# Kernel tuning notes

Hardware: AMD Instinct MI355X
Metric: run time of the kernel (lower is better)

Reference implementation:

```python
import jax, jax.numpy as jnp
import numpy as np

SLOPE = 25.0  # snntorch surrogate.fast_sigmoid default slope
THR = 1.0
BETA = 0.5
NUM_HEADS = 8

@jax.custom_vjp
def spike(u):
    # forward: heaviside; backward: fast-sigmoid surrogate
    return (u > 0).astype(u.dtype)

def _spike_fwd(u):
    return (u > 0).astype(u.dtype), u

def _spike_bwd(u, g):
    return (g / (SLOPE * jnp.abs(u) + 1.0) ** 2,)

spike.defvjp(_spike_fwd, _spike_bwd)

def lif(inp, mem):
    # snntorch Leaky, reset_mechanism='subtract': reset from previous mem (detached)
    reset = jax.lax.stop_gradient((mem > THR).astype(mem.dtype))
    mem_new = BETA * mem + inp - reset * THR
    spk = spike(mem_new - THR)
    return spk, mem_new

def conv1x1(x, W):
    # nn.Conv2d(C,C,1,bias=False): pure channel matmul
    return jnp.einsum('bihw,oi->bohw', x, W)

def setup_inputs():
    key = jax.random.key(0)
    ks = jax.random.split(key, 5)
    B, C, H, W = 8, 256, 64, 64
    x = jax.random.normal(ks[0], (B, C, H, W), jnp.float32)
    z = jnp.zeros((B, C, H, W), jnp.float32)
    s = 1.0 / np.sqrt(C)
    Wq = jax.random.normal(ks[1], (C, C), jnp.float32) * s
    Wk = jax.random.normal(ks[2], (C, C), jnp.float32) * s
    Wv = jax.random.normal(ks[3], (C, C), jnp.float32) * s
    Wo = jax.random.normal(ks[4], (C, C), jnp.float32) * s
    gamma = jnp.ones((C,), jnp.float32)
    beta_bn = jnp.zeros((C,), jnp.float32)
    return {'x': x, 'q_mem': z, 'k_mem': z, 'v_mem': z,
            'Wq': Wq, 'Wk': Wk, 'Wv': Wv, 'Wo': Wo,
            'gamma': gamma, 'beta_bn': beta_bn}

def reference(x, q_mem, k_mem, v_mem, Wq, Wk, Wv, Wo, gamma, beta_bn):
    B, C, H, W = x.shape
    N = H * W
    hd = C // NUM_HEADS
    scale = hd ** -0.5

    q_spk, q_mem_n = lif(conv1x1(x, Wq), q_mem)
    k_spk, k_mem_n = lif(conv1x1(x, Wk), k_mem)
    v_spk, v_mem_n = lif(conv1x1(x, Wv), v_mem)

    # bipolar spikes in {-1,+1}, reshape to (B, h, N, d)
    def to_heads(s):
        t = (2.0 * s - 1.0).reshape(B, NUM_HEADS, hd, N)
        return jnp.transpose(t, (0, 1, 3, 2))

    q = jax.nn.elu(to_heads(q_spk)) + 1.0
    k = jax.nn.elu(to_heads(k_spk)) + 1.0
    v = to_heads(v_spk)

    kv = jnp.einsum('bhnd,bhne->bhde', k, v)            # (B,h,d,d)
    out = jnp.einsum('bhnd,bhde->bhne', q, kv) * scale  # (B,h,N,d)
    k_sum = jnp.sum(k, axis=2)                          # (B,h,d)
    denom = jnp.einsum('bhnd,bhd->bhn', q, k_sum) + 1e-6
    out = out / denom[..., None]

    out = jnp.transpose(out, (0, 1, 3, 2)).reshape(B, C, H, W)
    out = conv1x1(out, Wo)

    # BatchNorm2d, training mode (biased batch stats), eps=1e-5
    mean = jnp.mean(out, axis=(0, 2, 3), keepdims=True)
    var = jnp.var(out, axis=(0, 2, 3), keepdims=True)
    out = (out - mean) / jnp.sqrt(var + 1e-5)
    out = out * gamma[None, :, None, None] + beta_bn[None, :, None, None]

    return (out, q_mem_n, k_mem_n, v_mem_n)
```

## Files before the change

### kernel.cpp

```cpp
#include <hip/hip_runtime.h>

#define B_ 8
#define C_ 256
#define N_ 4096
#define HD_ 32

#define ALPHA_ 0.36787944117144233f
#define BETAS_ (2.0f - ALPHA_)
#define SCALE_ 0.17677669529663687f

typedef _Float16 f16;
typedef _Float16 f16x8 __attribute__((ext_vector_type(8)));
typedef float f32x4 __attribute__((ext_vector_type(4)));

#define MFMA(a,b,c) __builtin_amdgcn_mfma_f32_16x16x32_f16((a),(b),(c),0,0,0)

#define GLDS(g, l) __builtin_amdgcn_global_load_lds( \
    (const __attribute__((address_space(1))) void*)(g), \
    (__attribute__((address_space(3))) void*)(l), 16, 0, 0)

__global__ __launch_bounds__(256) void transpose_split(
    const float* __restrict__ x, f16* __restrict__ XTh, f16* __restrict__ XTl)
{
    __shared__ float tile[32][257];
    int t = threadIdx.x;
    int b = blockIdx.z, i0 = blockIdx.y * 32, n0 = blockIdx.x * 256;
    const float* src = x + ((size_t)b * C_ + i0) * N_ + n0;
    int r = t >> 3, c0 = (t & 7) * 32;
    #pragma unroll
    for (int q = 0; q < 8; ++q) {
        float4 v = *reinterpret_cast<const float4*>(src + (size_t)r * N_ + c0 + q * 4);
        tile[r][c0 + q*4 + 0] = v.x; tile[r][c0 + q*4 + 1] = v.y;
        tile[r][c0 + q*4 + 2] = v.z; tile[r][c0 + q*4 + 3] = v.w;
    }
    __syncthreads();
    size_t ob = ((size_t)b * N_ + n0 + t) * C_ + i0;
    #pragma unroll
    for (int q = 0; q < 4; ++q) {
        f16x8 hv, lv;
        #pragma unroll
        for (int j = 0; j < 8; ++j) {
            float v = tile[q*8 + j][t];
            f16 h = (f16)v;
            hv[j] = h;
            lv[j] = (f16)(v - (float)h);
        }
        *reinterpret_cast<f16x8*>(XTh + ob + q*8) = hv;
        *reinterpret_cast<f16x8*>(XTl + ob + q*8) = lv;
    }
}

__global__ __launch_bounds__(256) void weight_split(
    const float* __restrict__ Wq, const float* __restrict__ Wk,
    const float* __restrict__ Wv, const float* __restrict__ Wo,
    f16* __restrict__ Wch, f16* __restrict__ Wcl)
{
    int idx4 = (blockIdx.x * 256 + threadIdx.x) * 4;
    int o = idx4 >> 8, i = idx4 & 255;
    const float* src = (o < 256) ? (Wq + (size_t)o * 256)
                     : (o < 512) ? (Wk + (size_t)(o - 256) * 256)
                     : (o < 768) ? (Wv + (size_t)(o - 512) * 256)
                                 : (Wo + (size_t)(o - 768) * 256);
    float4 v = *reinterpret_cast<const float4*>(src + i);
    f16 h0 = (f16)v.x, h1 = (f16)v.y, h2 = (f16)v.z, h3 = (f16)v.w;
    f16 hh[4] = { h0, h1, h2, h3 };
    f16 ll[4] = { (f16)(v.x - (float)h0), (f16)(v.y - (float)h1),
                  (f16)(v.z - (float)h2), (f16)(v.w - (float)h3) };
    *reinterpret_cast<uint2*>(Wch + idx4) = *reinterpret_cast<uint2*>(hh);
    *reinterpret_cast<uint2*>(Wcl + idx4) = *reinterpret_cast<uint2*>(ll);
}

template<int Y, bool LIF>
__global__ __launch_bounds__(256, 2) void mfma_gemm(
    const f16* __restrict__ Wch, const f16* __restrict__ Wcl,
    const f16* __restrict__ Bh,  const f16* __restrict__ Bl,
    const float* __restrict__ mq, const float* __restrict__ mk2,
    const float* __restrict__ mv,
    float* __restrict__ o0, float* __restrict__ o1, float* __restrict__ o2)
{
    int gid = blockIdx.x;
    int xcd = gid & 7, slot = gid >> 3;
    int y = slot % Y, gl = slot / Y;
    int b = xcd, xt = gl;
    int oBase = (LIF ? 0 : 768) + y * 128;
    int nT = xt * 256;

    const float* memP = nullptr; float* outP; int chBase;
    if (LIF) {
        int conv = y >> 1;
        memP = (conv == 0) ? mq : (conv == 1) ? mk2 : mv;
        outP = (conv == 0) ? o0 : (conv == 1) ? o1 : o2;
        chBase = (y & 1) * 128;
    } else { outP = o0; chBase = y * 128; }

    __shared__ f16 sm[3072 * 8];

    int t = threadIdx.x;
    int wid = t >> 6, lane = t & 63;
    int wm = wid >> 1, wn = wid & 1;
    int lr = lane & 15, g = lane >> 4;

    const f16* g0[12];
    #pragma unroll
    for (int i = 0; i < 12; ++i) {
        int s = wid * 768 + i * 64 + lane;
        const f16* gp;
        if (s < 512) {
            int r = s >> 2, c = (s & 3) ^ ((r >> 1) & 3);
            gp = Wch + (size_t)(oBase + r) * 256 + c * 8;
        } else if (s < 1024) {
            int s2 = s - 512; int r = s2 >> 2, c = (s2 & 3) ^ ((r >> 1) & 3);
            gp = Wcl + (size_t)(oBase + r) * 256 + c * 8;
        } else if (s < 2048) {
            int s2 = s - 1024; int r = s2 >> 2, c = (s2 & 3) ^ ((r >> 1) & 3);
            gp = Bh + ((size_t)b * N_ + nT + r) * 256 + c * 8;
        } else {
            int s2 = s - 2048; int r = s2 >> 2, c = (s2 & 3) ^ ((r >> 1) & 3);
            gp = Bl + ((size_t)b * N_ + nT + r) * 256 + c * 8;
        }
        g0[i] = gp;
    }

    f32x4 acc[4][8];
    #pragma unroll
    for (int m = 0; m < 4; ++m)
        #pragma unroll
        for (int n = 0; n < 8; ++n) acc[m][n] = (f32x4){0.f, 0.f, 0.f, 0.f};

    for (int k0 = 0; k0 < 256; k0 += 32) {
        #pragma unroll
        for (int i = 0; i < 12; ++i) {
            int s = wid * 768 + i * 64 + lane;
            GLDS(g0[i] + k0, &sm[s * 8]);
        }
        __syncthreads();

        f16x8 ah[4], al[4];
        #pragma unroll
        for (int m = 0; m < 4; ++m) {
            int r = wm * 64 + m * 16 + lr;
            int sw = g ^ ((r >> 1) & 3);
            ah[m] = *reinterpret_cast<const f16x8*>(&sm[(r * 4 + sw) * 8]);
            al[m] = *reinterpret_cast<const f16x8*>(&sm[(512 + r * 4 + sw) * 8]);
        }
        #pragma unroll
        for (int n = 0; n < 8; ++n) {
            int r = wn * 128 + n * 16 + lr;
            int sw = g ^ ((r >> 1) & 3);
            f16x8 bh8 = *reinterpret_cast<const f16x8*>(&sm[(1024 + r * 4 + sw) * 8]);
            f16x8 bl8 = *reinterpret_cast<const f16x8*>(&sm[(2048 + r * 4 + sw) * 8]);
            #pragma unroll
            for (int m = 0; m < 4; ++m) {
                acc[m][n] = MFMA(ah[m], bh8, acc[m][n]);
                acc[m][n] = MFMA(ah[m], bl8, acc[m][n]);
                acc[m][n] = MFMA(al[m], bh8, acc[m][n]);
            }
        }
        __syncthreads();
    }

    #pragma unroll
    for (int m = 0; m < 4; ++m) {
        int oLoc = chBase + wm * 64 + m * 16 + g * 4;
        #pragma unroll
        for (int n = 0; n < 8; ++n) {
            int nn = nT + wn * 128 + n * 16 + lr;
            #pragma unroll
            for (int r = 0; r < 4; ++r) {
                size_t idx = ((size_t)b * C_ + oLoc + r) * N_ + nn;
                float v = acc[m][n][r];
                if (LIF) {
                    float mm = memP[idx];
                    outP[idx] = 0.5f * mm + v - (mm > 1.0f ? 1.0f : 0.0f);
                } else {
                    outP[idx] = v;
                }
            }
        }
    }
}

__global__ __launch_bounds__(256) void kv_stage1(
    const float* __restrict__ Km, const float* __restrict__ Vm,
    int* __restrict__ pkv, int* __restrict__ pck, int* __restrict__ pcv)
{
    int bh = blockIdx.x, sl = blockIdx.y;
    int b = bh >> 3, h = bh & 7;
    const float* Kp = Km + ((size_t)(b * C_ + h * HD_)) * N_ + sl * 512;
    const float* Vp = Vm + ((size_t)(b * C_ + h * HD_)) * N_ + sl * 512;

    __shared__ unsigned long long mk[32][9], mv[32][9];
    int t = threadIdx.x, wave = t >> 6, lane = t & 63;

    for (int r = wave; r < 32; r += 4) {
        const float* kr = Kp + (size_t)r * N_;
        const float* vr = Vp + (size_t)r * N_;
        #pragma unroll
        for (int seg = 0; seg < 2; ++seg) {
            float4 kf = *reinterpret_cast<const float4*>(kr + seg * 256 + lane * 4);
            float4 vf = *reinterpret_cast<const float4*>(vr + seg * 256 + lane * 4);
            unsigned long long k0 = __ballot(kf.x > 1.0f);
            unsigned long long k1 = __ballot(kf.y > 1.0f);
            unsigned long long k2 = __ballot(kf.z > 1.0f);
            unsigned long long k3 = __ballot(kf.w > 1.0f);
            unsigned long long v0 = __ballot(vf.x > 1.0f);
            unsigned long long v1 = __ballot(vf.y > 1.0f);
            unsigned long long v2 = __ballot(vf.z > 1.0f);
            unsigned long long v3 = __ballot(vf.w > 1.0f);
            if (lane == 0) {
                mk[r][seg*4+0] = k0; mk[r][seg*4+1] = k1;
                mk[r][seg*4+2] = k2; mk[r][seg*4+3] = k3;
                mv[r][seg*4+0] = v0; mv[r][seg*4+1] = v1;
                mv[r][seg*4+2] = v2; mv[r][seg*4+3] = v3;
            }
        }
    }
    __syncthreads();

    int base = (bh * 8 + sl);
    int d = t >> 3, e0 = (t & 7) * 4;
    #pragma unroll
    for (int j = 0; j < 4; ++j) {
        int e = e0 + j, P = 0;
        #pragma unroll
        for (int w = 0; w < 8; ++w) P += __popcll(mk[d][w] & mv[e][w]);
        pkv[(size_t)base * 1024 + d * 32 + e] = P;
    }
    if (t < 32) {
        int c = 0;
        #pragma unroll
        for (int w = 0; w < 8; ++w) c += __popcll(mk[t][w]);
        pck[base * 32 + t] = c;
    } else if (t < 64) {
        int dd = t - 32, c = 0;
        #pragma unroll
        for (int w = 0; w < 8; ++w) c += __popcll(mv[dd][w]);
        pcv[base * 32 + dd] = c;
    }
}

__global__ __launch_bounds__(256) void kv_stage2(
    const int* __restrict__ pkv, const int* __restrict__ pck,
    const int* __restrict__ pcv, float* __restrict__ kvp, float* __restrict__ ksump)
{
    int bh = blockIdx.x, t = threadIdx.x;
    __shared__ float ck[32], cv[32];
    if (t < 32) {
        int s = 0;
        #pragma unroll
        for (int sl = 0; sl < 8; ++sl) s += pck[(bh * 8 + sl) * 32 + t];
        ck[t] = (float)s;
    } else if (t < 64) {
        int dd = t - 32, s = 0;
        #pragma unroll
        for (int sl = 0; sl < 8; ++sl) s += pcv[(bh * 8 + sl) * 32 + dd];
        cv[dd] = (float)s;
    }
    __syncthreads();
    int d = t >> 3, e0 = (t & 7) * 4;
    #pragma unroll
    for (int j = 0; j < 4; ++j) {
        int e = e0 + j, P = 0;
        #pragma unroll
        for (int sl = 0; sl < 8; ++sl) P += pkv[(size_t)(bh * 8 + sl) * 1024 + d * 32 + e];
        float skv = 2.0f * (float)P - ck[d];
        float sv  = 2.0f * cv[e] - 4096.0f;
        kvp[(size_t)bh * 1024 + d * 32 + e] = ALPHA_ * sv + BETAS_ * skv;
    }
    if ((t & 7) == 0)
        ksump[bh * 32 + d] = ALPHA_ * 4096.0f + BETAS_ * ck[d];
}

__global__ __launch_bounds__(256) void att_kernel(
    const float* __restrict__ Qm, const float* __restrict__ kvp,
    const float* __restrict__ ksump, f16* __restrict__ ATh, f16* __restrict__ ATl)
{
    int bh = blockIdx.y; int b = bh >> 3, h = bh & 7;
    int n0 = blockIdx.x * 256;
    const float* Qp = Qm + ((size_t)(b * C_ + h * HD_)) * N_;

    __shared__ float qs[32][260];
    int t = threadIdx.x;
    {
        int r  = t >> 3, c0 = (t & 7) * 32;
        #pragma unroll
        for (int q4 = 0; q4 < 8; ++q4) {
            float4 v = *reinterpret_cast<const float4*>(&Qp[(size_t)r * N_ + n0 + c0 + q4 * 4]);
            qs[r][c0 + q4*4 + 0] = (v.x > 1.0f) ? 2.0f : ALPHA_;
            qs[r][c0 + q4*4 + 1] = (v.y > 1.0f) ? 2.0f : ALPHA_;
            qs[r][c0 + q4*4 + 2] = (v.z > 1.0f) ? 2.0f : ALPHA_;
            qs[r][c0 + q4*4 + 3] = (v.w > 1.0f) ? 2.0f : ALPHA_;
        }
    }
    __syncthreads();

    float q[32];
    #pragma unroll
    for (int d2 = 0; d2 < 32; ++d2) q[d2] = qs[d2][t];

    const float* ksb = ksump + bh * 32;
    float den = 1e-6f;
    #pragma unroll
    for (int d2 = 0; d2 < 32; ++d2) den += q[d2] * ksb[d2];
    float rden = SCALE_ / den;

    const float* kvb = kvp + (size_t)bh * 1024;
    size_t ob = ((size_t)b * N_ + n0 + t) * C_ + h * HD_;
    #pragma unroll
    for (int qq = 0; qq < 4; ++qq) {
        f16x8 hv, lv;
        #pragma unroll
        for (int j = 0; j < 8; ++j) {
            int e = qq * 8 + j;
            float num = 0.0f;
            #pragma unroll
            for (int d2 = 0; d2 < 32; ++d2) num += q[d2] * kvb[d2 * 32 + e];
            float val = num * rden;
            f16 hh = (f16)val;
            hv[j] = hh;
            lv[j] = (f16)(val - (float)hh);
        }
        *reinterpret_cast<f16x8*>(ATh + ob + qq * 8) = hv;
        *reinterpret_cast<f16x8*>(ATl + ob + qq * 8) = lv;
    }
}

__global__ __launch_bounds__(1024) void bn_stats(
    const float* __restrict__ out2, float* __restrict__ stats)
{
    int o = blockIdx.x, t = threadIdx.x;
    double s = 0.0, ss = 0.0;
    for (int b = 0; b < B_; ++b) {
        const float* p = out2 + ((size_t)b * C_ + o) * N_;
        float4 v = *reinterpret_cast<const float4*>(&p[t * 4]);
        s  += (double)v.x + (double)v.y + (double)v.z + (double)v.w;
        ss += (double)v.x * v.x + (double)v.y * v.y + (double)v.z * v.z + (double)v.w * v.w;
    }
    __shared__ double rs[1024], rss[1024];
    rs[t] = s; rss[t] = ss;
    __syncthreads();
    for (int st = 512; st > 0; st >>= 1) {
        if (t < st) { rs[t] += rs[t + st]; rss[t] += rss[t + st]; }
        __syncthreads();
    }
    if (t == 0) {
        double mean = rs[0] / 32768.0;
        double var  = rss[0] / 32768.0 - mean * mean;
        stats[o * 2 + 0] = (float)mean;
        stats[o * 2 + 1] = (float)(1.0 / sqrt(var + 1e-5));
    }
}

__global__ __launch_bounds__(256) void bn_apply(
    float* __restrict__ out, const float* __restrict__ stats,
    const float* __restrict__ gamma, const float* __restrict__ beta)
{
    size_t i = ((size_t)blockIdx.x * 256 + threadIdx.x) * 4;
    int o = (int)((i >> 12) & 255);
    float m = stats[o * 2], r = stats[o * 2 + 1];
    float g = gamma[o] * r;
    float c = beta[o] - m * g;
    float4 v = *reinterpret_cast<float4*>(&out[i]);
    v.x = v.x * g + c; v.y = v.y * g + c;
    v.z = v.z * g + c; v.w = v.w * g + c;
    *reinterpret_cast<float4*>(&out[i]) = v;
}

extern "C" void kernel_launch(void* const* d_in, const int* in_sizes, int n_in,
                              void* d_out, int out_size, void* d_ws, size_t ws_size,
                              hipStream_t stream)
{
    (void)in_sizes; (void)n_in; (void)out_size; (void)ws_size;

    const float* x     = (const float*)d_in[0];
    const float* qmem  = (const float*)d_in[1];
    const float* kmem  = (const float*)d_in[2];
    const float* vmem  = (const float*)d_in[3];
    const float* Wq    = (const float*)d_in[4];
    const float* Wk    = (const float*)d_in[5];
    const float* Wv    = (const float*)d_in[6];
    const float* Wo    = (const float*)d_in[7];
    const float* gamma = (const float*)d_in[8];
    const float* beta  = (const float*)d_in[9];

    const size_t TSZ = (size_t)B_ * C_ * N_;
    float* out0 = (float*)d_out;
    float* outq = out0 + TSZ;
    float* outk = outq + TSZ;
    float* outv = outk + TSZ;

    char* w = (char*)d_ws;
    f16* XTh = (f16*)w;           w += TSZ * 2;
    f16* XTl = (f16*)w;           w += TSZ * 2;
    f16* ATh = (f16*)w;           w += TSZ * 2;
    f16* ATl = (f16*)w;           w += TSZ * 2;
    f16* Wch = (f16*)w;           w += 1024 * 256 * 2;
    f16* Wcl = (f16*)w;           w += 1024 * 256 * 2;
    int* pkv = (int*)w;           w += 64 * 8 * 1024 * 4;
    int* pck = (int*)w;           w += 64 * 8 * 32 * 4;
    int* pcv = (int*)w;           w += 64 * 8 * 32 * 4;
    float* kvp   = (float*)w;     w += 64 * 1024 * 4;
    float* ksump = (float*)w;     w += 64 * 32 * 4;
    float* stats = (float*)w;     w += 256 * 2 * 4;

    dim3 blk(256);

    transpose_split<<<dim3(16, 8, 8), blk, 0, stream>>>(x, XTh, XTl);
    weight_split<<<dim3(256), blk, 0, stream>>>(Wq, Wk, Wv, Wo, Wch, Wcl);

    mfma_gemm<6, true><<<dim3(768), blk, 0, stream>>>(
        Wch, Wcl, XTh, XTl, qmem, kmem, vmem, outq, outk, outv);

    kv_stage1<<<dim3(64, 8), blk, 0, stream>>>(outk, outv, pkv, pck, pcv);
    kv_stage2<<<dim3(64), blk, 0, stream>>>(pkv, pck, pcv, kvp, ksump);

    att_kernel<<<dim3(16, 64), blk, 0, stream>>>(outq, kvp, ksump, ATh, ATl);

    mfma_gemm<2, false><<<dim3(256), blk, 0, stream>>>(
        Wch, Wcl, ATh, ATl, nullptr, nullptr, nullptr, out0, nullptr, nullptr);

    bn_stats<<<dim3(256), dim3(1024), 0, stream>>>(out0, stats);
    bn_apply<<<dim3(8192), blk, 0, stream>>>(out0, stats, gamma, beta);
}
```

Baseline: 184.6 us.

## Double-buffer LDS in split-f16 MFMA GEMM and retile to 256x128 with 512 threads

The GEMM kernel now keeps two LDS buffers and issues global-to-LDS loads for the next K slice while computing on the current one, which removes one barrier per iteration and hides load latency. The tile shape changes from 128 output channels x 256 pixels with 256 threads to 256 channels x 128 pixels with 512 threads (8 waves), halving each wave's accumulator count. The grid mapping changes accordingly (one conv per y). In exchange, LDS use doubles to about 96KB per block, so only one block fits per CU. The loop also still has a trailing barrier, and whether the single barrier is enough to guard the buffer being overwritten depends on how it is placed.

```diff
diff --git a/kernel.cpp b/kernel.cpp
--- a/kernel.cpp
+++ b/kernel.cpp
@@ -71,7 +71,7 @@
 }
 
 template<int Y, bool LIF>
-__global__ __launch_bounds__(256, 2) void mfma_gemm(
+__global__ __launch_bounds__(512, 1) void mfma_gemm(
     const f16* __restrict__ Wch, const f16* __restrict__ Wcl,
     const f16* __restrict__ Bh,  const f16* __restrict__ Bl,
     const float* __restrict__ mq, const float* __restrict__ mk2,
@@ -79,76 +79,83 @@
     float* __restrict__ o0, float* __restrict__ o1, float* __restrict__ o2)
 {
     int gid = blockIdx.x;
-    int xcd = gid & 7, slot = gid >> 3;
-    int y = slot % Y, gl = slot / Y;
-    int b = xcd, xt = gl;
-    int oBase = (LIF ? 0 : 768) + y * 128;
-    int nT = xt * 256;
-
-    const float* memP = nullptr; float* outP; int chBase;
+    int b = gid & 7, slot = gid >> 3;
+    int y = slot % Y, nt = slot / Y;
+    int oBase = LIF ? y * 256 : 768;
+    int nT = nt * 128;
+
+    const float* memP = nullptr; float* outP;
     if (LIF) {
-        int conv = y >> 1;
-        memP = (conv == 0) ? mq : (conv == 1) ? mk2 : mv;
-        outP = (conv == 0) ? o0 : (conv == 1) ? o1 : o2;
-        chBase = (y & 1) * 128;
-    } else { outP = o0; chBase = y * 128; }
-
-    __shared__ f16 sm[3072 * 8];
+        memP = (y == 0) ? mq : (y == 1) ? mk2 : mv;
+        outP = (y == 0) ? o0 : (y == 1) ? o1 : o2;
+    } else outP = o0;
+
+    __shared__ __align__(16) f16 sm[2][3072 * 8];
 
     int t = threadIdx.x;
     int wid = t >> 6, lane = t & 63;
     int wm = wid >> 1, wn = wid & 1;
     int lr = lane & 15, g = lane >> 4;
 
-    const f16* g0[12];
-    #pragma unroll
-    for (int i = 0; i < 12; ++i) {
-        int s = wid * 768 + i * 64 + lane;
+    const f16* g0[6];
+    #pragma unroll
+    for (int i = 0; i < 6; ++i) {
+        int s = i * 512 + t;
         const f16* gp;
-        if (s < 512) {
+        if (s < 1024) {
             int r = s >> 2, c = (s & 3) ^ ((r >> 1) & 3);
             gp = Wch + (size_t)(oBase + r) * 256 + c * 8;
-        } else if (s < 1024) {
-            int s2 = s - 512; int r = s2 >> 2, c = (s2 & 3) ^ ((r >> 1) & 3);
-            gp = Wcl + (size_t)(oBase + r) * 256 + c * 8;
         } else if (s < 2048) {
             int s2 = s - 1024; int r = s2 >> 2, c = (s2 & 3) ^ ((r >> 1) & 3);
+            gp = Wcl + (size_t)(oBase + r) * 256 + c * 8;
+        } else if (s < 2560) {
+            int s2 = s - 2048; int r = s2 >> 2, c = (s2 & 3) ^ ((r >> 1) & 3);
             gp = Bh + ((size_t)b * N_ + nT + r) * 256 + c * 8;
         } else {
-            int s2 = s - 2048; int r = s2 >> 2, c = (s2 & 3) ^ ((r >> 1) & 3);
+            int s2 = s - 2560; int r = s2 >> 2, c = (s2 & 3) ^ ((r >> 1) & 3);
             gp = Bl + ((size_t)b * N_ + nT + r) * 256 + c * 8;
         }
         g0[i] = gp;
     }
 
-    f32x4 acc[4][8];
+    f32x4 acc[4][4];
     #pragma unroll
     for (int m = 0; m < 4; ++m)
         #pragma unroll
-        for (int n = 0; n < 8; ++n) acc[m][n] = (f32x4){0.f, 0.f, 0.f, 0.f};
-
-    for (int k0 = 0; k0 < 256; k0 += 32) {
-        #pragma unroll
-        for (int i = 0; i < 12; ++i) {
-            int s = wid * 768 + i * 64 + lane;
-            GLDS(g0[i] + k0, &sm[s * 8]);
-        }
-        __syncthreads();
-
+        for (int n = 0; n < 4; ++n) acc[m][n] = (f32x4){0.f, 0.f, 0.f, 0.f};
+
+    #pragma unroll
+    for (int i = 0; i < 6; ++i) {
+        int s = i * 512 + t;
+        GLDS(g0[i], &sm[0][s * 8]);
+    }
+    __syncthreads();
+
+    for (int ks = 0; ks < 8; ++ks) {
+        int cur = ks & 1;
+        if (ks < 7) {
+            int k = (ks + 1) * 32;
+            #pragma unroll
+            for (int i = 0; i < 6; ++i) {
+                int s = i * 512 + t;
+                GLDS(g0[i] + k, &sm[cur ^ 1][s * 8]);
+            }
+        }
+        const f16* smc = sm[cur];
         f16x8 ah[4], al[4];
         #pragma unroll
         for (int m = 0; m < 4; ++m) {
             int r = wm * 64 + m * 16 + lr;
             int sw = g ^ ((r >> 1) & 3);
-            ah[m] = *reinterpret_cast<const f16x8*>(&sm[(r * 4 + sw) * 8]);
-            al[m] = *reinterpret_cast<const f16x8*>(&sm[(512 + r * 4 + sw) * 8]);
-        }
-        #pragma unroll
-        for (int n = 0; n < 8; ++n) {
-            int r = wn * 128 + n * 16 + lr;
-            int sw = g ^ ((r >> 1) & 3);
-            f16x8 bh8 = *reinterpret_cast<const f16x8*>(&sm[(1024 + r * 4 + sw) * 8]);
-            f16x8 bl8 = *reinterpret_cast<const f16x8*>(&sm[(2048 + r * 4 + sw) * 8]);
+            ah[m] = *reinterpret_cast<const f16x8*>(&smc[(r * 4 + sw) * 8]);
+            al[m] = *reinterpret_cast<const f16x8*>(&smc[(1024 + r * 4 + sw) * 8]);
+        }
+        #pragma unroll
+        for (int n = 0; n < 4; ++n) {
+            int rb = wn * 64 + n * 16 + lr;
+            int sw = g ^ ((rb >> 1) & 3);
+            f16x8 bh8 = *reinterpret_cast<const f16x8*>(&smc[(2048 + rb * 4 + sw) * 8]);
+            f16x8 bl8 = *reinterpret_cast<const f16x8*>(&smc[(2560 + rb * 4 + sw) * 8]);
             #pragma unroll
             for (int m = 0; m < 4; ++m) {
                 acc[m][n] = MFMA(ah[m], bh8, acc[m][n]);
@@ -161,10 +168,10 @@
 
     #pragma unroll
     for (int m = 0; m < 4; ++m) {
-        int oLoc = chBase + wm * 64 + m * 16 + g * 4;
-        #pragma unroll
-        for (int n = 0; n < 8; ++n) {
-            int nn = nT + wn * 128 + n * 16 + lr;
+        int oLoc = wm * 64 + m * 16 + g * 4;
+        #pragma unroll
+        for (int n = 0; n < 4; ++n) {
+            int nn = nT + wn * 64 + n * 16 + lr;
             #pragma unroll
             for (int r = 0; r < 4; ++r) {
                 size_t idx = ((size_t)b * C_ + oLoc + r) * N_ + nn;
@@ -408,7 +415,7 @@
     transpose_split<<<dim3(16, 8, 8), blk, 0, stream>>>(x, XTh, XTl);
     weight_split<<<dim3(256), blk, 0, stream>>>(Wq, Wk, Wv, Wo, Wch, Wcl);
 
-    mfma_gemm<6, true><<<dim3(768), blk, 0, stream>>>(
+    mfma_gemm<3, true><<<dim3(768), dim3(512), 0, stream>>>(
         Wch, Wcl, XTh, XTl, qmem, kmem, vmem, outq, outk, outv);
 
     kv_stage1<<<dim3(64, 8), blk, 0, stream>>>(outk, outv, pkv, pck, pcv);
@@ -416,7 +423,7 @@
 
     att_kernel<<<dim3(16, 64), blk, 0, stream>>>(outq, kvp, ksump, ATh, ATl);
 
-    mfma_gemm<2, false><<<dim3(256), blk, 0, stream>>>(
+    mfma_gemm<1, false><<<dim3(256), dim3(512), 0, stream>>>(
         Wch, Wcl, ATh, ATl, nullptr, nullptr, nullptr, out0, nullptr, nullptr);
 
     bn_stats<<<dim3(256), dim3(1024), 0, stream>>>(out0, stats);
```

New measurement: 235.8 us. 1.28x slower.
